# Kernel optimization log

Measured on AMD Instinct MI355X. Metric: run time of the kernel, lower is better.

The kernel has to match this reference:

```python
import jax, jax.numpy as jnp
import numpy as np

S, B, H = 2048, 2, 2048
NH = 16
HD = H // NH
SCALE = HD ** -0.5


def setup_inputs() -> dict:
    key = jax.random.key(0)
    ks = jax.random.split(key, 5)
    sigma = 0.02
    return {
        "x": jax.random.normal(ks[0], (S, B, H), dtype=jnp.float32),
        "wq": jax.random.normal(ks[1], (H, H), dtype=jnp.float32) * sigma,
        "wk": jax.random.normal(ks[2], (H, H), dtype=jnp.float32) * sigma,
        "wv": jax.random.normal(ks[3], (H, H), dtype=jnp.float32) * sigma,
        "wo": jax.random.normal(ks[4], (H, H), dtype=jnp.float32) * sigma,
    }


def reference(x, wq, wk, wv, wo):
    # x: [s, b, h]; F.linear(x, W) == x @ W.T
    q = x @ wq.T
    k = x @ wk.T
    v = x @ wv.T
    s, b, _ = q.shape
    # [s, b, h] -> [b, nh, s, hd]
    def split_heads(t):
        return t.reshape(s, b, NH, HD).transpose(1, 2, 0, 3)
    q, k, v = split_heads(q), split_heads(k), split_heads(v)
    scores = jnp.einsum("bhqd,bhkd->bhqk", q, k) * SCALE
    attn = jax.nn.softmax(scores.astype(jnp.float32), axis=-1).astype(q.dtype)
    out = jnp.einsum("bhqk,bhkd->bhqd", attn, v)
    # [b, nh, s, hd] -> [s, b, h]
    out = out.transpose(2, 0, 1, 3).reshape(s, b, NH * HD)
    return out @ wo.T
```

## Files before the change

kernel.cpp:

```cpp
#include <hip/hip_runtime.h>

typedef __bf16 bf16;
typedef __bf16 bf16x8 __attribute__((ext_vector_type(8)));
typedef float f32x4 __attribute__((ext_vector_type(4)));
typedef float f32x16 __attribute__((ext_vector_type(16)));
typedef unsigned int uint;

#define GLOAD16(g, l)                                                        \
  __builtin_amdgcn_global_load_lds(                                          \
      (const __attribute__((address_space(1))) void*)(g),                    \
      (__attribute__((address_space(3))) void*)(l), 16, 0, 0)

__device__ inline uint pack_bf16(float a, float b) {
  union { bf16 h[2]; uint u; } x;
  x.h[0] = (bf16)a; x.h[1] = (bf16)b;
  return x.u;
}

__global__ void cast_f32_to_bf16(const float* __restrict__ in,
                                 bf16* __restrict__ out, int n8, float scale) {
  int i = blockIdx.x * blockDim.x + threadIdx.x;
  if (i >= n8) return;
  const float4* p = reinterpret_cast<const float4*>(in) + (size_t)i * 2;
  float4 a = p[0], b = p[1];
  bf16x8 o;
  o[0] = (bf16)(a.x * scale); o[1] = (bf16)(a.y * scale);
  o[2] = (bf16)(a.z * scale); o[3] = (bf16)(a.w * scale);
  o[4] = (bf16)(b.x * scale); o[5] = (bf16)(b.y * scale);
  o[6] = (bf16)(b.z * scale); o[7] = (bf16)(b.w * scale);
  *reinterpret_cast<bf16x8*>(out + (size_t)i * 8) = o;
}

template <typename OT>
__global__ __launch_bounds__(512, 2) void gemm_nt_256(
    const bf16* __restrict__ A, const bf16* __restrict__ B, OT* __restrict__ C,
    int K, int lda, int ldb, int ldc, long bsB, long bsC) {
  extern __shared__ char sh[];
  const int t = threadIdx.x;
  const int w = t >> 6, lane = t & 63;
  const int l15 = lane & 15, l4 = lane >> 4;
  const int wr = w >> 1, wc = w & 1;
  const int m0 = blockIdx.y * 256;
  const int n0 = blockIdx.x * 128;
  const bf16* Bg = B + (size_t)blockIdx.z * bsB;
  OT* Cg = C + (size_t)blockIdx.z * bsC;

  int sRow[4], sCol[4];
#pragma unroll
  for (int i = 0; i < 4; i++) {
    int sB_ = (i * 512 + t) * 16;
    int row = sB_ >> 7;
    int ge = (sB_ ^ ((row & 7) << 4)) >> 1;
    sRow[i] = ge >> 6;
    sCol[i] = ge & 63;
  }

  const int NT = K >> 6;
  f32x4 acc[4][4] = {};

  auto stage = [&](int tt) {
    char* dst = sh + (size_t)(tt % 3) * 49152;
    const int k0 = tt * 64;
#pragma unroll
    for (int i = 0; i < 4; i++)
      GLOAD16(A + (size_t)(m0 + sRow[i]) * lda + k0 + sCol[i],
              dst + (i * 512 + w * 64) * 16);
#pragma unroll
    for (int i = 0; i < 2; i++)
      GLOAD16(Bg + (size_t)(n0 + sRow[i]) * ldb + k0 + sCol[i],
              dst + 32768 + (i * 512 + w * 64) * 16);
  };

  auto compute = [&](int tt) {
    const char* Ab = sh + (size_t)(tt % 3) * 49152;
    const char* Bb = Ab + 32768;
    bf16x8 bfr[4][2];
#pragma unroll
    for (int n = 0; n < 4; n++)
#pragma unroll
      for (int kk = 0; kk < 2; kk++) {
        int row = wc * 64 + n * 16 + l15;
        int off = (row * 128 + kk * 64 + l4 * 16) ^ ((row & 7) << 4);
        bfr[n][kk] = *reinterpret_cast<const bf16x8*>(Bb + off);
      }
#pragma unroll
    for (int mh = 0; mh < 2; mh++) {
      bf16x8 af[2][2];
#pragma unroll
      for (int m = 0; m < 2; m++)
#pragma unroll
        for (int kk = 0; kk < 2; kk++) {
          int row = wr * 64 + (mh * 2 + m) * 16 + l15;
          int off = (row * 128 + kk * 64 + l4 * 16) ^ ((row & 7) << 4);
          af[m][kk] = *reinterpret_cast<const bf16x8*>(Ab + off);
        }
      __builtin_amdgcn_s_setprio(1);
#pragma unroll
      for (int m = 0; m < 2; m++)
#pragma unroll
        for (int n = 0; n < 4; n++)
#pragma unroll
          for (int kk = 0; kk < 2; kk++)
            acc[mh * 2 + m][n] = __builtin_amdgcn_mfma_f32_16x16x32_bf16(
                af[m][kk], bfr[n][kk], acc[mh * 2 + m][n], 0, 0, 0);
      __builtin_amdgcn_s_setprio(0);
    }
  };

  stage(0);
  stage(1);
  for (int tt = 0; tt < NT - 1; ++tt) {
    asm volatile("s_waitcnt vmcnt(6)" ::: "memory");
    __builtin_amdgcn_s_barrier();
    if (tt + 2 < NT) stage(tt + 2);
    compute(tt);
  }
  asm volatile("s_waitcnt vmcnt(0)" ::: "memory");
  __builtin_amdgcn_s_barrier();
  compute(NT - 1);

#pragma unroll
  for (int m = 0; m < 4; m++)
#pragma unroll
    for (int n = 0; n < 4; n++)
#pragma unroll
      for (int j = 0; j < 4; j++) {
        int row = m0 + wr * 64 + m * 16 + l4 * 4 + j;
        int col = n0 + wc * 64 + n * 16 + l15;
        Cg[(size_t)row * ldc + col] = (OT)acc[m][n][j];
      }
}

__global__ __launch_bounds__(256, 2) void attn_fwd(
    const bf16* __restrict__ Q, const bf16* __restrict__ Kb,
    const bf16* __restrict__ Vt, bf16* __restrict__ O) {
  __shared__ bf16 Ks[2][64 * 128];
  __shared__ bf16 Vs[2][64 * 128];
  const int t = threadIdx.x, w = t >> 6, lane = t & 63;
  const int l31 = lane & 31, half = lane >> 5;
  const int bh = blockIdx.x;
  const int b = bh >> 4, h = bh & 15;
  const int sq0 = blockIdx.y * 128 + w * 32;
  const size_t hoff = (size_t)h * 128;
  const size_t bO = (size_t)b * 2048 + hoff;

  bf16x8 qf[8];
  {
    const bf16* qp = Q + ((size_t)(sq0 + l31) * 2 + b) * 2048 + hoff + half * 8;
#pragma unroll
    for (int dc = 0; dc < 8; dc++)
      qf[dc] = *reinterpret_cast<const bf16x8*>(qp + dc * 16);
  }

  const bf16* kp[4];
  const bf16* vp[4];
#pragma unroll
  for (int i = 0; i < 4; i++) {
    int s = i * 256 + t;
    int row = s >> 4, g = s & 15;
    int lg = g ^ (row & 15);
    kp[i] = Kb + ((size_t)row * 2 + b) * 2048 + hoff + lg * 8;
    int d = row * 2 + (lg >> 3);
    vp[i] = Vt + (bO + d) * 2048 + (lg & 7) * 8;
  }

  auto stage = [&](int nb, int sk0) {
#pragma unroll
    for (int i = 0; i < 4; i++)
      GLOAD16(kp[i] + (size_t)sk0 * 4096, Ks[nb] + (i * 256 + w * 64) * 8);
#pragma unroll
    for (int i = 0; i < 4; i++)
      GLOAD16(vp[i] + sk0, Vs[nb] + (i * 256 + w * 64) * 8);
  };

  f32x16 acc_o[4] = {};
  float m_run = -3e38f, l_run = 0.f;

  stage(0, 0);

  for (int it = 0; it < 32; ++it) {
    const int cur = it & 1;
    __syncthreads();
    if (it + 1 < 32) stage(cur ^ 1, (it + 1) * 64);

    const char* ksb = reinterpret_cast<const char*>(Ks[cur]);
    const char* vsb = reinterpret_cast<const char*>(Vs[cur]);

    f32x16 sc[2] = {};
    __builtin_amdgcn_s_setprio(1);
#pragma unroll
    for (int dc = 0; dc < 8; dc++) {
      int kx = ((dc * 2 + half) ^ (l31 & 15)) << 4;
#pragma unroll
      for (int kt = 0; kt < 2; kt++) {
        int kB = ((kt * 32 + l31) << 8) + kx;
        bf16x8 kf = *reinterpret_cast<const bf16x8*>(ksb + kB);
        sc[kt] = __builtin_amdgcn_mfma_f32_32x32x16_bf16(kf, qf[dc], sc[kt], 0, 0, 0);
      }
    }
    __builtin_amdgcn_s_setprio(0);

    float pmax = -3e38f;
#pragma unroll
    for (int kt = 0; kt < 2; kt++)
#pragma unroll
      for (int r = 0; r < 16; r++) pmax = fmaxf(pmax, sc[kt][r]);
    pmax = fmaxf(pmax, __shfl_xor(pmax, 32));

    if (!__all(pmax - m_run <= 11.0f)) {
      float mn = fmaxf(m_run, pmax);
      float f = exp2f(m_run - mn);
      m_run = mn;
      l_run *= f;
#pragma unroll
      for (int idx = 0; idx < 16; idx++) {
        float fr = __shfl(f, (idx & 3) + 8 * (idx >> 2) + half * 4);
#pragma unroll
        for (int dcb = 0; dcb < 4; dcb++) acc_o[dcb][idx] *= fr;
      }
    }

    float rs = 0.f;
#pragma unroll
    for (int kt = 0; kt < 2; kt++)
#pragma unroll
      for (int r = 0; r < 16; r++) {
        float p = exp2f(sc[kt][r] - m_run);
        sc[kt][r] = p;
        rs += p;
      }
    rs += __shfl_xor(rs, 32);
    l_run += rs;

    uint pa[4][4];
#pragma unroll
    for (int skc = 0; skc < 4; skc++) {
      int kt = skc >> 1, s8 = (skc & 1) * 8;
      uint pk01 = pack_bf16(sc[kt][s8 + 0], sc[kt][s8 + 1]);
      uint pk23 = pack_bf16(sc[kt][s8 + 2], sc[kt][s8 + 3]);
      uint pk45 = pack_bf16(sc[kt][s8 + 4], sc[kt][s8 + 5]);
      uint pk67 = pack_bf16(sc[kt][s8 + 6], sc[kt][s8 + 7]);
      uint o01 = __shfl_xor(pk01, 32), o23 = __shfl_xor(pk23, 32);
      uint o45 = __shfl_xor(pk45, 32), o67 = __shfl_xor(pk67, 32);
      pa[skc][0] = half ? o45 : pk01;
      pa[skc][1] = half ? o67 : pk23;
      pa[skc][2] = half ? pk45 : o01;
      pa[skc][3] = half ? pk67 : o23;
    }

    __builtin_amdgcn_s_setprio(1);
#pragma unroll
    for (int dcb = 0; dcb < 4; dcb++) {
      int rp = dcb * 16 + (l31 >> 1);
      int pbit = (l31 & 1) << 3;
#pragma unroll
      for (int skc = 0; skc < 4; skc++) {
        int vB = (rp << 8) + (((pbit + skc * 2 + half) ^ (l31 >> 1)) << 4);
        bf16x8 vf = *reinterpret_cast<const bf16x8*>(vsb + vB);
        union { uint u[4]; bf16x8 v; } af;
        af.u[0] = pa[skc][0]; af.u[1] = pa[skc][1];
        af.u[2] = pa[skc][2]; af.u[3] = pa[skc][3];
        acc_o[dcb] = __builtin_amdgcn_mfma_f32_32x32x16_bf16(af.v, vf, acc_o[dcb], 0, 0, 0);
      }
    }
    __builtin_amdgcn_s_setprio(0);
  }

  float inv = 1.0f / l_run;
#pragma unroll
  for (int idx = 0; idx < 16; idx++) {
    int sr = (idx & 3) + 8 * (idx >> 2) + half * 4;
    float invr = __shfl(inv, sr);
    bf16* op = O + ((size_t)(sq0 + sr) * 2 + b) * 2048 + hoff + l31;
#pragma unroll
    for (int dcb = 0; dcb < 4; dcb++)
      op[dcb * 32] = (bf16)(acc_o[dcb][idx] * invr);
  }
}

extern "C" void kernel_launch(void* const* d_in, const int* in_sizes, int n_in,
                              void* d_out, int out_size, void* d_ws,
                              size_t ws_size, hipStream_t stream) {
  (void)in_sizes; (void)n_in; (void)out_size; (void)ws_size;
  const float* x  = (const float*)d_in[0];
  const float* wq = (const float*)d_in[1];
  const float* wk = (const float*)d_in[2];
  const float* wv = (const float*)d_in[3];
  const float* wo = (const float*)d_in[4];
  float* out = (float*)d_out;
  char* ws = (char*)d_ws;
  bf16* xb   = (bf16*)(ws);
  bf16* qb   = (bf16*)(ws + (1u << 24));
  bf16* kb   = (bf16*)(ws + (2u << 24));
  bf16* vt   = (bf16*)(ws + (3u << 24));
  bf16* wb   = (bf16*)(ws + (4u << 24));
  bf16* attn = xb;
  const float SCALE = 0.08838834764831845f * 1.4426950408889634f;
  const int SMEM = 3 * 49152;

  hipFuncSetAttribute((const void*)gemm_nt_256<bf16>,
                      hipFuncAttributeMaxDynamicSharedMemorySize, SMEM);
  hipFuncSetAttribute((const void*)gemm_nt_256<float>,
                      hipFuncAttributeMaxDynamicSharedMemorySize, SMEM);

  cast_f32_to_bf16<<<4096, 256, 0, stream>>>(x, xb, 8388608 / 8, 1.0f);

  dim3 g1(16, 16, 1);
  cast_f32_to_bf16<<<2048, 256, 0, stream>>>(wq, wb, 4194304 / 8, SCALE);
  gemm_nt_256<bf16><<<g1, 512, SMEM, stream>>>(xb, wb, qb, 2048, 2048, 2048, 2048, 0, 0);

  cast_f32_to_bf16<<<2048, 256, 0, stream>>>(wk, wb, 4194304 / 8, 1.0f);
  gemm_nt_256<bf16><<<g1, 512, SMEM, stream>>>(xb, wb, kb, 2048, 2048, 2048, 2048, 0, 0);

  cast_f32_to_bf16<<<2048, 256, 0, stream>>>(wv, wb, 4194304 / 8, 1.0f);
  dim3 g2(16, 8, 2);
  gemm_nt_256<bf16><<<g2, 512, SMEM, stream>>>(wb, xb, vt, 2048, 2048, 4096, 2048,
                                               2048L, 4194304L);

  dim3 ga(32, 16);
  attn_fwd<<<ga, 256, 0, stream>>>(qb, kb, vt, attn);

  cast_f32_to_bf16<<<2048, 256, 0, stream>>>(wo, wb, 4194304 / 8, 1.0f);
  gemm_nt_256<float><<<g1, 512, SMEM, stream>>>(attn, wb, out, 2048, 2048, 2048, 2048, 0, 0);
}
```

Before: 272.7 us.

## Swizzle GEMM block order and prefetch K/V fragments into registers in attention

The GEMM kernel remaps its linear block id so consecutive workgroups are spread across groups of eight, aiming at better L2 locality across XCDs. The attention loop now loads all K fragments from LDS into registers before the QK MFMAs, and loads all V fragments before the softmax so the LDS reads overlap the softmax math. The row max and row sum reductions become tree reductions to shorten dependency chains. Register pressure goes up by 32 bf16x8 values, which may reduce occupancy or cause spills.

```diff
diff --git a/kernel.cpp b/kernel.cpp
--- a/kernel.cpp
+++ b/kernel.cpp
@@ -40,8 +40,13 @@
   const int w = t >> 6, lane = t & 63;
   const int l15 = lane & 15, l4 = lane >> 4;
   const int wr = w >> 1, wc = w & 1;
-  const int m0 = blockIdx.y * 256;
-  const int n0 = blockIdx.x * 128;
+  const int gx = gridDim.x, gy = gridDim.y;
+  const int nwg = gx * gy;
+  const int bid = blockIdx.y * gx + blockIdx.x;
+  const int fid = (bid & 7) * (nwg >> 3) + (bid >> 3);
+  const int by = fid / gx, bx = fid - by * gx;
+  const int m0 = by * 256;
+  const int n0 = bx * 128;
   const bf16* Bg = B + (size_t)blockIdx.z * bsB;
   OT* Cg = C + (size_t)blockIdx.z * bsC;
 
@@ -186,26 +191,44 @@
     const char* ksb = reinterpret_cast<const char*>(Ks[cur]);
     const char* vsb = reinterpret_cast<const char*>(Vs[cur]);
 
+    bf16x8 kf[16];
+#pragma unroll
+    for (int dc = 0; dc < 8; dc++) {
+      int kx = ((dc * 2 + half) ^ (l31 & 15)) << 4;
+#pragma unroll
+      for (int kt = 0; kt < 2; kt++)
+        kf[kt * 8 + dc] = *reinterpret_cast<const bf16x8*>(
+            ksb + ((kt * 32 + l31) << 8) + kx);
+    }
+
     f32x16 sc[2] = {};
     __builtin_amdgcn_s_setprio(1);
 #pragma unroll
     for (int dc = 0; dc < 8; dc++) {
-      int kx = ((dc * 2 + half) ^ (l31 & 15)) << 4;
-#pragma unroll
-      for (int kt = 0; kt < 2; kt++) {
-        int kB = ((kt * 32 + l31) << 8) + kx;
-        bf16x8 kf = *reinterpret_cast<const bf16x8*>(ksb + kB);
-        sc[kt] = __builtin_amdgcn_mfma_f32_32x32x16_bf16(kf, qf[dc], sc[kt], 0, 0, 0);
-      }
+      sc[0] = __builtin_amdgcn_mfma_f32_32x32x16_bf16(kf[dc], qf[dc], sc[0], 0, 0, 0);
+      sc[1] = __builtin_amdgcn_mfma_f32_32x32x16_bf16(kf[8 + dc], qf[dc], sc[1], 0, 0, 0);
     }
     __builtin_amdgcn_s_setprio(0);
 
-    float pmax = -3e38f;
-#pragma unroll
-    for (int kt = 0; kt < 2; kt++)
-#pragma unroll
-      for (int r = 0; r < 16; r++) pmax = fmaxf(pmax, sc[kt][r]);
-    pmax = fmaxf(pmax, __shfl_xor(pmax, 32));
+    bf16x8 vf[16];
+#pragma unroll
+    for (int dcb = 0; dcb < 4; dcb++) {
+      int rp = dcb * 16 + (l31 >> 1);
+      int pbit = (l31 & 1) << 3;
+#pragma unroll
+      for (int skc = 0; skc < 4; skc++)
+        vf[dcb * 4 + skc] = *reinterpret_cast<const bf16x8*>(
+            vsb + (rp << 8) + (((pbit + skc * 2 + half) ^ (l31 >> 1)) << 4));
+    }
+
+    float red[16];
+#pragma unroll
+    for (int r = 0; r < 16; r++) red[r] = fmaxf(sc[0][r], sc[1][r]);
+#pragma unroll
+    for (int s = 8; s >= 1; s >>= 1)
+#pragma unroll
+      for (int r = 0; r < s; r++) red[r] = fmaxf(red[r], red[r + s]);
+    float pmax = fmaxf(red[0], __shfl_xor(red[0], 32));
 
     if (!__all(pmax - m_run <= 11.0f)) {
       float mn = fmaxf(m_run, pmax);
@@ -220,16 +243,17 @@
       }
     }
 
-    float rs = 0.f;
 #pragma unroll
     for (int kt = 0; kt < 2; kt++)
 #pragma unroll
-      for (int r = 0; r < 16; r++) {
-        float p = exp2f(sc[kt][r] - m_run);
-        sc[kt][r] = p;
-        rs += p;
-      }
-    rs += __shfl_xor(rs, 32);
+      for (int r = 0; r < 16; r++) sc[kt][r] = exp2f(sc[kt][r] - m_run);
+#pragma unroll
+    for (int r = 0; r < 16; r++) red[r] = sc[0][r] + sc[1][r];
+#pragma unroll
+    for (int s = 8; s >= 1; s >>= 1)
+#pragma unroll
+      for (int r = 0; r < s; r++) red[r] += red[r + s];
+    float rs = red[0] + __shfl_xor(red[0], 32);
     l_run += rs;
 
     uint pa[4][4];
@@ -251,16 +275,13 @@
     __builtin_amdgcn_s_setprio(1);
 #pragma unroll
     for (int dcb = 0; dcb < 4; dcb++) {
-      int rp = dcb * 16 + (l31 >> 1);
-      int pbit = (l31 & 1) << 3;
 #pragma unroll
       for (int skc = 0; skc < 4; skc++) {
-        int vB = (rp << 8) + (((pbit + skc * 2 + half) ^ (l31 >> 1)) << 4);
-        bf16x8 vf = *reinterpret_cast<const bf16x8*>(vsb + vB);
         union { uint u[4]; bf16x8 v; } af;
         af.u[0] = pa[skc][0]; af.u[1] = pa[skc][1];
         af.u[2] = pa[skc][2]; af.u[3] = pa[skc][3];
-        acc_o[dcb] = __builtin_amdgcn_mfma_f32_32x32x16_bf16(af.v, vf, acc_o[dcb], 0, 0, 0);
+        acc_o[dcb] = __builtin_amdgcn_mfma_f32_32x32x16_bf16(
+            af.v, vf[dcb * 4 + skc], acc_o[dcb], 0, 0, 0);
       }
     }
     __builtin_amdgcn_s_setprio(0);
```

New measurement: 283.3 us. 1.04x slower.
